# Performance work log

Hardware: AMD Instinct MI355X
Metric: run time of the kernel (lower is better)

Reference implementation:

```python
import jax, jax.numpy as jnp
import numpy as np

HS_LIST = [1024, 2048]   # hidden_size choices
IS_LIST = [2752, 5504]   # intermediate_size choices
A_BITS = [4, 8]
W_BITS = [4, 8]


def fake_quant(t, bits):
    # symmetric per-tensor fake quantization with straight-through estimator
    qmax = 2.0 ** (bits - 1) - 1.0
    s = jnp.maximum(jnp.max(jnp.abs(t)) / qmax, 1e-8)
    q = jnp.round(t / s) * s
    return t + jax.lax.stop_gradient(q - t)


def mixed_linear(inp, W, in_sizes, out_sizes, p_in, p_out, p_a, p_w):
    """Weight-entangled mixed-precision linear: weighted sum over the
    cartesian product of (in_size, out_size, a_bit, w_bit) choices.
    W has shape [max(out_sizes), max(in_sizes)]; sub-slices are shared."""
    out_max = max(out_sizes)
    acc = jnp.zeros(inp.shape[:-1] + (out_max,), inp.dtype)
    for i, cin in enumerate(in_sizes):
        x_sub = inp[..., :cin]
        for k, ab in enumerate(A_BITS):
            xq = fake_quant(x_sub, ab)
            for j, cout in enumerate(out_sizes):
                w_sub = W[:cout, :cin]
                for l, wb in enumerate(W_BITS):
                    wq = fake_quant(w_sub, wb)
                    y = jnp.einsum('bsh,oh->bso', xq, wq)
                    y = jnp.pad(y, ((0, 0), (0, 0), (0, out_max - cout)))
                    acc = acc + (p_in[i] * p_out[j] * p_a[k] * p_w[l]) * y
    return acc


def setup_inputs() -> dict:
    key = jax.random.key(0)
    ks = jax.random.split(key, 8)
    HS, IS = max(HS_LIST), max(IS_LIST)
    return {
        'x': jax.random.normal(ks[0], (1, 1024, HS), jnp.float32),
        'p_hidden': jax.random.normal(ks[1], (2,), jnp.float32),
        'p_inter': jax.random.normal(ks[2], (2,), jnp.float32),
        'p_abit': jax.random.normal(ks[3], (2,), jnp.float32),
        'p_wbit': jax.random.normal(ks[4], (2,), jnp.float32),
        'W_gate': jax.random.normal(ks[5], (IS, HS), jnp.float32) * 0.02,
        'W_up': jax.random.normal(ks[6], (IS, HS), jnp.float32) * 0.02,
        'W_down': jax.random.normal(ks[7], (HS, IS), jnp.float32) * 0.02,
    }


def reference(x, p_hidden, p_inter, p_abit, p_wbit, W_gate, W_up, W_down):
    # mixop softmaxes the architecture parameters into mixture probabilities
    wh = jax.nn.softmax(p_hidden)
    wi = jax.nn.softmax(p_inter)
    wa = jax.nn.softmax(p_abit)
    ww = jax.nn.softmax(p_wbit)
    x_up = mixed_linear(x, W_up, HS_LIST, IS_LIST, wh, wi, wa, ww)
    x_gate = jax.nn.silu(mixed_linear(x, W_gate, HS_LIST, IS_LIST, wh, wi, wa, ww))
    h = x_gate * x_up
    # down_proj (reverse=True): input dims are intermediate, output dims hidden;
    # op list is built over (intermediate, hidden) choices, weighted in the same
    # arch-param order (hidden probs pair with the first/intermediate choice axis).
    out = mixed_linear(h, W_down, IS_LIST, HS_LIST, wh, wi, wa, ww)
    return out
```

## Files before the change

kernel.cpp:

```cpp
#include <hip/hip_runtime.h>

typedef __attribute__((ext_vector_type(8))) short short8;
typedef __attribute__((ext_vector_type(4))) float f32x4;
typedef unsigned short u16;
typedef unsigned int u32;
typedef unsigned long long u64;

#define P_WH 0
#define P_WI 2
#define P_WA 4
#define P_WW 6
#define SL_AX 8
#define SL_WUP 12
#define SL_WGATE 16
#define SL_WDOWN 20
#define SL_AH 24
#define P_SX 28
#define P_SWUP 32
#define P_SWGATE 40
#define P_SWDOWN 48
#define P_SH 56

__device__ __forceinline__ u16 f2bf(float f) {
  u32 u = __float_as_uint(f);
  u = (u + 0x7FFFu + ((u >> 16) & 1u)) >> 16;
  return (u16)u;
}
__device__ __forceinline__ float bf2f(u16 h) { return __uint_as_float(((u32)h) << 16); }
__device__ __forceinline__ float fquant(float v, float s) { return rintf(v / s) * s; }

typedef const __attribute__((address_space(1))) u32 gl_u32;
typedef __attribute__((address_space(3))) u32 lds_u32;
__device__ __forceinline__ void gload_lds16(const void* g, void* l) {
  __builtin_amdgcn_global_load_lds((gl_u32*)g, (lds_u32*)l, 16, 0, 0);
}

#define WAITVM8()  asm volatile("s_waitcnt vmcnt(8)" ::: "memory")
#define WAITVM2()  asm volatile("s_waitcnt vmcnt(2)" ::: "memory")
#define WAITVM0()  asm volatile("s_waitcnt vmcnt(0)" ::: "memory")
#define BARRIER()  asm volatile("s_barrier" ::: "memory")

__global__ void k_init(const float* ph, const float* pi, const float* pa,
                       const float* pw, float* P) {
  if (threadIdx.x == 0) {
    u32* U = (u32*)P;
    for (int i = SL_AX; i < SL_AH + 2; ++i) U[i] = 0u;
    const float* src[4] = {ph, pi, pa, pw};
    #pragma unroll
    for (int t = 0; t < 4; ++t) {
      float a = src[t][0], b = src[t][1];
      float mx = fmaxf(a, b);
      float ea = expf(a - mx), eb = expf(b - mx);
      float s = ea + eb;
      P[t * 2 + 0] = ea / s;
      P[t * 2 + 1] = eb / s;
    }
  }
}

template <bool POW2>
__device__ __forceinline__ void amax_proc(float4 d, int v, u32 magic, int C,
                                          int r0, int c0,
                                          float& m0, float& m1, float& m2, float& m3) {
  int lin = v << 2;
  int o, c;
  if (POW2) { o = lin >> 11; c = lin & 2047; }
  else {
    o = (int)(((u64)(u32)lin * magic) >> 40);
    c = lin - o * C;
  }
  float mm = fmaxf(fmaxf(fabsf(d.x), fabsf(d.y)), fmaxf(fabsf(d.z), fabsf(d.w)));
  bool rlo = o < r0, clo = c < c0;
  m0 = fmaxf(m0, (rlo && clo) ? mm : 0.f);
  m1 = fmaxf(m1, (rlo && !clo) ? mm : 0.f);
  m2 = fmaxf(m2, (!rlo && clo) ? mm : 0.f);
  m3 = fmaxf(m3, (!rlo && !clo) ? mm : 0.f);
}

template <bool POW2>
__device__ __forceinline__ void absmax_dev(const float4* __restrict__ A4,
                                           int nvec, u32 magic, int C, int r0, int c0,
                                           int slotbase, float* P, int bid, int nb) {
  float m0 = 0.f, m1 = 0.f, m2 = 0.f, m3 = 0.f;
  const int tid = threadIdx.x;
  const int step = nb * 256;
  int v = bid * 256 + tid;
  for (; v + 3 * step < nvec; v += 4 * step) {
    float4 d0 = A4[v];
    float4 d1 = A4[v + step];
    float4 d2 = A4[v + 2 * step];
    float4 d3 = A4[v + 3 * step];
    amax_proc<POW2>(d0, v,            magic, C, r0, c0, m0, m1, m2, m3);
    amax_proc<POW2>(d1, v + step,     magic, C, r0, c0, m0, m1, m2, m3);
    amax_proc<POW2>(d2, v + 2 * step, magic, C, r0, c0, m0, m1, m2, m3);
    amax_proc<POW2>(d3, v + 3 * step, magic, C, r0, c0, m0, m1, m2, m3);
  }
  for (; v < nvec; v += step) {
    float4 d0 = A4[v];
    amax_proc<POW2>(d0, v, magic, C, r0, c0, m0, m1, m2, m3);
  }
  #pragma unroll
  for (int off = 32; off > 0; off >>= 1) {
    m0 = fmaxf(m0, __shfl_xor(m0, off));
    m1 = fmaxf(m1, __shfl_xor(m1, off));
    m2 = fmaxf(m2, __shfl_xor(m2, off));
    m3 = fmaxf(m3, __shfl_xor(m3, off));
  }
  __shared__ float red[16];
  const int wave = tid >> 6;
  if ((tid & 63) == 0) {
    red[wave * 4 + 0] = m0;
    red[wave * 4 + 1] = m1;
    red[wave * 4 + 2] = m2;
    red[wave * 4 + 3] = m3;
  }
  __syncthreads();
  if (tid < 4) {
    float mm = fmaxf(fmaxf(red[tid], red[4 + tid]), fmaxf(red[8 + tid], red[12 + tid]));
    if (mm > 0.f) atomicMax((u32*)P + slotbase + tid, __float_as_uint(mm));
  }
}

__global__ __launch_bounds__(256) void k_absmax4(const float* x, const float* Wu,
                                                 const float* Wg, const float* Wd,
                                                 u32 magic5504, float* P) {
  int b = blockIdx.x;
  if (b < 256)        absmax_dev<true >((const float4*)x,  (1024 * 2048) >> 2, 0, 2048, 1024, 1024, SL_AX,    P, b,        256);
  else if (b < 768)   absmax_dev<true >((const float4*)Wu, (5504 * 2048) >> 2, 0, 2048, 2752, 1024, SL_WUP,   P, b - 256,  512);
  else if (b < 1280)  absmax_dev<true >((const float4*)Wg, (5504 * 2048) >> 2, 0, 2048, 2752, 1024, SL_WGATE, P, b - 768,  512);
  else                absmax_dev<false>((const float4*)Wd, (2048 * 5504) >> 2, magic5504, 5504, 1024, 2752, SL_WDOWN, P, b - 1280, 512);
}

__global__ void k_params1(float* P) {
  if (threadIdx.x != 0 || blockIdx.x != 0) return;
  u32* U = (u32*)P;
  float x00 = __uint_as_float(U[SL_AX + 0]);
  float x01 = __uint_as_float(U[SL_AX + 1]);
  float ax0 = x00;
  float ax1 = fmaxf(x00, x01);
  P[P_SX + 0] = fmaxf(ax0 / 7.f, 1e-8f);
  P[P_SX + 1] = fmaxf(ax0 / 127.f, 1e-8f);
  P[P_SX + 2] = fmaxf(ax1 / 7.f, 1e-8f);
  P[P_SX + 3] = fmaxf(ax1 / 127.f, 1e-8f);
  const int sl[3] = {SL_WUP, SL_WGATE, SL_WDOWN};
  const int sb[3] = {P_SWUP, P_SWGATE, P_SWDOWN};
  #pragma unroll
  for (int t = 0; t < 3; ++t) {
    float q00 = __uint_as_float(U[sl[t] + 0]);
    float q01 = __uint_as_float(U[sl[t] + 1]);
    float q10 = __uint_as_float(U[sl[t] + 2]);
    float q11 = __uint_as_float(U[sl[t] + 3]);
    float a0 = q00;
    float a1 = fmaxf(q00, q10);
    float a2 = fmaxf(q00, q01);
    float a3 = fmaxf(fmaxf(q00, q01), fmaxf(q10, q11));
    float aa[4] = {a0, a1, a2, a3};
    #pragma unroll
    for (int ij = 0; ij < 4; ++ij) {
      P[sb[t] + ij * 2 + 0] = fmaxf(aa[ij] / 7.f, 1e-8f);
      P[sb[t] + ij * 2 + 1] = fmaxf(aa[ij] / 127.f, 1e-8f);
    }
  }
}

__global__ void k_params2(float* P) {
  if (threadIdx.x != 0 || blockIdx.x != 0) return;
  u32* U = (u32*)P;
  float a0 = __uint_as_float(U[SL_AH]);
  float a1 = fmaxf(a0, __uint_as_float(U[SL_AH + 1]));
  P[P_SH + 0] = fmaxf(a0 / 7.f, 1e-8f);
  P[P_SH + 1] = fmaxf(a0 / 127.f, 1e-8f);
  P[P_SH + 2] = fmaxf(a1 / 7.f, 1e-8f);
  P[P_SH + 3] = fmaxf(a1 / 127.f, 1e-8f);
}

__device__ __forceinline__ void build_x_one(
    const float* __restrict__ src, const float* __restrict__ P,
    u16* __restrict__ Xh, u16* __restrict__ Xl,
    int Csrc, int cin0, int K, int sbx, int gid, int kpr) {
  int row = gid / kpr;
  int kc_out = (gid - row * kpr) << 3;
  int kc_log = kc_out ^ (((row >> 1) & 3) << 3);
  int i = (kc_log >= cin0) ? 1 : 0;
  int c = kc_log - i * cin0;
  float pin = P[P_WH + i];
  float wa0 = P[P_WA], wa1 = P[P_WA + 1];
  float s4 = P[sbx + i * 2], s8 = P[sbx + i * 2 + 1];
  const float* sp = src + (size_t)row * Csrc + c;
  float v[8];
  *(float4*)&v[0] = *(const float4*)sp;
  *(float4*)&v[4] = *(const float4*)(sp + 4);
  short8 hv, lv;
  #pragma unroll
  for (int e = 0; e < 8; ++e) {
    float val = pin * (wa0 * fquant(v[e], s4) + wa1 * fquant(v[e], s8));
    u16 h = f2bf(val);
    hv[e] = (short)h;
    lv[e] = (short)f2bf(val - bf2f(h));
  }
  size_t off = (size_t)row * K + kc_out;
  *(short8*)(Xh + off) = hv;
  *(short8*)(Xl + off) = lv;
}

__device__ __forceinline__ void build_w_one(
    const float* __restrict__ W, const float* __restrict__ P,
    u16* __restrict__ Wh, u16* __restrict__ Wl,
    int Csrc, int cin0, int K, int sbw, int cout0, int rowoff,
    int gid, int kpr) {
  int row = gid / kpr;
  int kc_out = (gid - row * kpr) << 3;
  int kc_log = kc_out ^ (((row >> 1) & 3) << 3);
  int i = (kc_log >= cin0) ? 1 : 0;
  int c = kc_log - i * cin0;
  float wi0 = P[P_WI], wi1 = P[P_WI + 1];
  float ww0 = P[P_WW], ww1 = P[P_WW + 1];
  float s00 = P[sbw + i * 4 + 0];
  float s01 = P[sbw + i * 4 + 1];
  float s10 = P[sbw + i * 4 + 2];
  float s11 = P[sbw + i * 4 + 3];
  float keep0 = (row < cout0) ? wi0 : 0.f;
  const float* sp = W + (size_t)row * Csrc + c;
  float v[8];
  *(float4*)&v[0] = *(const float4*)sp;
  *(float4*)&v[4] = *(const float4*)(sp + 4);
  short8 hv, lv;
  #pragma unroll
  for (int e = 0; e < 8; ++e) {
    float w = v[e];
    float t0 = ww0 * fquant(w, s00) + ww1 * fquant(w, s01);
    float t1 = ww0 * fquant(w, s10) + ww1 * fquant(w, s11);
    float val = keep0 * t0 + wi1 * t1;
    u16 h = f2bf(val);
    hv[e] = (short)h;
    lv[e] = (short)f2bf(val - bf2f(h));
  }
  size_t off = (size_t)(row + rowoff) * K + kc_out;
  *(short8*)(Wh + off) = hv;
  *(short8*)(Wl + off) = lv;
}

__global__ __launch_bounds__(256) void k_build_x(
    const float* __restrict__ src, const float* __restrict__ P,
    u16* __restrict__ Xh, u16* __restrict__ Xl,
    int rows, int Csrc, int cin0, int K, int sbx) {
  int kpr = K >> 3;
  int nch = rows * kpr;
  int gid = blockIdx.x * blockDim.x + threadIdx.x;
  if (gid >= nch) return;
  build_x_one(src, P, Xh, Xl, Csrc, cin0, K, sbx, gid, kpr);
}

__global__ __launch_bounds__(256) void k_build_w(
    const float* __restrict__ W, const float* __restrict__ P,
    u16* __restrict__ Wh, u16* __restrict__ Wl,
    int R, int Csrc, int cin0, int K, int sbw, int cout0) {
  int kpr = K >> 3;
  int nch = R * kpr;
  int gid = blockIdx.x * blockDim.x + threadIdx.x;
  if (gid >= nch) return;
  build_w_one(W, P, Wh, Wl, Csrc, cin0, K, sbw, cout0, 0, gid, kpr);
}

__global__ __launch_bounds__(256) void k_build1(
    const float* __restrict__ x, const float* __restrict__ Wu,
    const float* __restrict__ Wg, const float* __restrict__ P,
    u16* __restrict__ X1h, u16* __restrict__ X1l,
    u16* __restrict__ Wh, u16* __restrict__ Wl) {
  int bid = blockIdx.x;
  if (bid < 1536) {
    int gid = bid * 256 + threadIdx.x;
    build_x_one(x, P, X1h, X1l, 2048, 1024, 3072, P_SX, gid, 384);
  } else {
    int gid = (bid - 1536) * 256 + threadIdx.x;
    const int nch = 5504 * 384;
    if (gid < nch)
      build_w_one(Wu, P, Wh, Wl, 2048, 1024, 3072, P_SWUP,   2752, 0,    gid,       384);
    else
      build_w_one(Wg, P, Wh, Wl, 2048, 1024, 3072, P_SWGATE, 2752, 5504, gid - nch, 384);
  }
}

__global__ __launch_bounds__(256) void k_build2(
    const float* __restrict__ H, const float* __restrict__ Wd,
    const float* __restrict__ P,
    u16* __restrict__ X2h, u16* __restrict__ X2l,
    u16* __restrict__ Wdh, u16* __restrict__ Wdl) {
  int bid = blockIdx.x;
  if (bid < 4128) {
    int gid = bid * 256 + threadIdx.x;
    build_x_one(H, P, X2h, X2l, 5504, 2752, 8256, P_SH, gid, 1032);
  } else {
    int gid = (bid - 4128) * 256 + threadIdx.x;
    build_w_one(Wd, P, Wdh, Wdl, 5504, 2752, 8256, P_SWDOWN, 1024, 0, gid, 1032);
  }
}

__global__ __launch_bounds__(256) void k_h(const float* __restrict__ U_,
                                           const float* __restrict__ G_,
                                           float* __restrict__ H_, float* P) {
  int nvec = (1024 * 5504) >> 2;
  int gstride = gridDim.x * blockDim.x;
  float m0 = 0.f, m1 = 0.f;
  for (int v = blockIdx.x * blockDim.x + threadIdx.x; v < nvec; v += gstride) {
    float4 u = ((const float4*)U_)[v];
    float4 g = ((const float4*)G_)[v];
    float4 h;
    h.x = u.x * (g.x / (1.f + expf(-g.x)));
    h.y = u.y * (g.y / (1.f + expf(-g.y)));
    h.z = u.z * (g.z / (1.f + expf(-g.z)));
    h.w = u.w * (g.w / (1.f + expf(-g.w)));
    ((float4*)H_)[v] = h;
    int c = (v << 2) % 5504;
    float mm = fmaxf(fmaxf(fabsf(h.x), fabsf(h.y)), fmaxf(fabsf(h.z), fabsf(h.w)));
    if (c < 2752) m0 = fmaxf(m0, mm); else m1 = fmaxf(m1, mm);
  }
  #pragma unroll
  for (int off = 32; off > 0; off >>= 1) {
    m0 = fmaxf(m0, __shfl_xor(m0, off));
    m1 = fmaxf(m1, __shfl_xor(m1, off));
  }
  if ((threadIdx.x & 63) == 0) {
    u32* slots = (u32*)P;
    if (m0 > 0.f) atomicMax(slots + SL_AH, __float_as_uint(m0));
    if (m1 > 0.f) atomicMax(slots + SL_AH + 1, __float_as_uint(m1));
  }
}

template <int MF, int NF>
__global__ __launch_bounds__(256) void k_gemm(
    const u16* __restrict__ Ah, const u16* __restrict__ Al,
    const u16* __restrict__ Bh, const u16* __restrict__ Bl,
    float* __restrict__ C0, float* __restrict__ C1, int nsplit, int ldc,
    int M, int N, int K) {
  constexpr int BM = MF * 32;
  constexpr int BN = NF * 32;
  constexpr int HALF = (2 * BM + 2 * BN) * 32;
  constexpr int nsegA = BM / 16;
  constexpr int nsegB = BN / 16;
  constexpr int NSEG = 2 * nsegA + 2 * nsegB;
  constexpr int NJ = NSEG / 4;
  static_assert(NJ == 8, "vmcnt immediates assume 8 loads per stage");
  __shared__ __align__(16) u16 S[2 * HALF];

  const int tid = threadIdx.x;
  const int wave = tid >> 6;
  const int lane = tid & 63;

  const int gx = gridDim.x;
  const int nwg = gx * gridDim.y;
  const int orig = blockIdx.y * gx + blockIdx.x;
  const int q = nwg >> 3, r = nwg & 7;
  const int xcd = orig & 7, linb = orig >> 3;
  const int swz = (xcd < r ? xcd * (q + 1) : r * (q + 1) + (xcd - r) * q) + linb;
  const int m0 = (swz % gx) * BM;
  const int n0 = (swz / gx) * BN;

  const int St = K >> 5;
  const int Z = gridDim.z;
  const int zb = St / Z, zr = St - zb * Z;
  const int z = blockIdx.z;
  const int nst = zb + ((z < zr) ? 1 : 0);
  const int k0 = (z * zb + ((z < zr) ? z : zr)) << 5;

  const int wr = wave >> 1, wc = wave & 1;
  const int lrow = lane >> 2;
  const int lcol = (lane & 3) << 3;
  const int fr = lane & 15;
  const int fq4 = (lane >> 4) << 2;
  const int kofs = (lane >> 4) << 3;

  f32x4 acc[MF][NF];
  #pragma unroll
  for (int m = 0; m < MF; ++m)
    #pragma unroll
    for (int n = 0; n < NF; ++n) acc[m][n] = (f32x4){0.f, 0.f, 0.f, 0.f};

  const u16* srcp[NJ];
  int loff[NJ];
  #pragma unroll
  for (int j = 0; j < NJ; ++j) {
    int g = j * 4 + wave;
    const u16* gb; int abase, trow, segi;
    if (g < nsegA)               { gb = Ah; abase = 0;                  trow = m0; segi = g; }
    else if (g < 2 * nsegA)      { gb = Al; abase = BM * 32;            trow = m0; segi = g - nsegA; }
    else if (g < 2 * nsegA + nsegB) { gb = Bh; abase = 2 * BM * 32;     trow = n0; segi = g - 2 * nsegA; }
    else                         { gb = Bl; abase = 2 * BM * 32 + BN * 32; trow = n0; segi = g - 2 * nsegA - nsegB; }
    srcp[j] = gb + (size_t)(trow + segi * 16 + lrow) * K + (k0 + lcol);
    loff[j] = abase + segi * 512;
  }

  int aoh[MF], aol[MF], boh[NF], bol[NF];
  #pragma unroll
  for (int m = 0; m < MF; ++m) {
    int rr = wr * (MF * 16) + m * 16 + fr;
    int idx = rr * 32 + (kofs ^ (((rr >> 1) & 3) << 3));
    aoh[m] = idx;
    aol[m] = BM * 32 + idx;
  }
  #pragma unroll
  for (int n = 0; n < NF; ++n) {
    int rr = wc * (NF * 16) + n * 16 + fr;
    int idx = rr * 32 + (kofs ^ (((rr >> 1) & 3) << 3));
    boh[n] = 2 * BM * 32 + idx;
    bol[n] = 2 * BM * 32 + BN * 32 + idx;
  }

  #define STAGE(bufo)                                           \
    { _Pragma("unroll")                                         \
      for (int j = 0; j < NJ; ++j) {                            \
        gload_lds16(srcp[j], S + (bufo) + loff[j]);             \
        srcp[j] += 32;                                          \
      } }

  #define COMPUTE(bufo)                                                         \
    { short8 afh[MF], afl[MF], bfh[NF], bfl[NF];                                \
      _Pragma("unroll")                                                         \
      for (int m = 0; m < MF; ++m) {                                            \
        afh[m] = *(const short8*)(S + (bufo) + aoh[m]);                         \
        afl[m] = *(const short8*)(S + (bufo) + aol[m]);                         \
      }                                                                         \
      _Pragma("unroll")                                                         \
      for (int n = 0; n < NF; ++n) {                                            \
        bfh[n] = *(const short8*)(S + (bufo) + boh[n]);                         \
        bfl[n] = *(const short8*)(S + (bufo) + bol[n]);                         \
      }                                                                         \
      _Pragma("unroll")                                                         \
      for (int m = 0; m < MF; ++m)                                              \
        _Pragma("unroll")                                                       \
        for (int n = 0; n < NF; ++n) {                                          \
          acc[m][n] = __builtin_amdgcn_mfma_f32_16x16x32_bf16(afh[m], bfh[n], acc[m][n], 0, 0, 0); \
          acc[m][n] = __builtin_amdgcn_mfma_f32_16x16x32_bf16(afh[m], bfl[n], acc[m][n], 0, 0, 0); \
          acc[m][n] = __builtin_amdgcn_mfma_f32_16x16x32_bf16(afl[m], bfh[n], acc[m][n], 0, 0, 0); \
        } }

  int curo = 0;
  STAGE(curo);
  for (int t = 0; t + 1 < nst; ++t) {
    STAGE(curo ^ HALF);
    WAITVM8();
    BARRIER();
    COMPUTE(curo);
    BARRIER();
    curo ^= HALF;
  }
  WAITVM0();
  BARRIER();
  COMPUTE(curo);

  #undef STAGE
  #undef COMPUTE

  float* base = (n0 < nsplit) ? C0 : C1;
  const int ncol0 = (n0 < nsplit) ? 0 : nsplit;
  float* Cz = base + (size_t)z * M * ldc;
  #pragma unroll
  for (int m = 0; m < MF; ++m) {
    #pragma unroll
    for (int n = 0; n < NF; ++n) {
      int row = m0 + wr * (MF * 16) + m * 16 + fq4;
      int col = n0 + wc * (NF * 16) + n * 16 + fr - ncol0;
      float* cp = Cz + (size_t)row * ldc + col;
      f32x4 a = acc[m][n];
      cp[0] = a[0];
      cp[(size_t)ldc] = a[1];
      cp[(size_t)2 * ldc] = a[2];
      cp[(size_t)3 * ldc] = a[3];
    }
  }
}

template <int CMODE>
__global__ __launch_bounds__(512) void k_gemm8w(
    const u16* __restrict__ Ah, const u16* __restrict__ Al,
    const u16* __restrict__ Bh, const u16* __restrict__ Bl,
    float* __restrict__ C0, float* __restrict__ C1, int nsplit, int ldc,
    int M, int N, int K) {
  constexpr int BM = 256, BN = 256;
  constexpr int HALF = (2 * BM + 2 * BN) * 32;
  constexpr int NJ = 8;
  __shared__ __align__(16) u16 S[2 * HALF];

  const int tid = threadIdx.x;
  const int wave = tid >> 6;
  const int lane = tid & 63;

  const int gx = gridDim.x;
  const int nwg = gx * gridDim.y;
  const int orig = blockIdx.y * gx + blockIdx.x;
  const int q = nwg >> 3, r = nwg & 7;
  const int xcd = orig & 7, linb = orig >> 3;
  const int swz = (xcd < r ? xcd * (q + 1) : r * (q + 1) + (xcd - r) * q) + linb;
  const int m0 = (swz % gx) * BM;
  const int n0 = (swz / gx) * BN;

  const int St = K >> 5;
  const int Z = gridDim.z;
  const int zb = St / Z, zr = St - zb * Z;
  const int z = blockIdx.z;
  const int nst = zb + ((z < zr) ? 1 : 0);
  const int k0 = (z * zb + ((z < zr) ? z : zr)) << 5;

  const int wr = wave >> 2;
  const int wc = wave & 3;
  const int lrow = lane >> 2;
  const int lcol = (lane & 3) << 3;
  const int fr = lane & 15;
  const int fq4 = (lane >> 4) << 2;
  const int kofs = (lane >> 4) << 3;
  const int kx = kofs ^ (((fr >> 1) & 3) << 3);

  f32x4 acc[8][4];
  #pragma unroll
  for (int m = 0; m < 8; ++m)
    #pragma unroll
    for (int n = 0; n < 4; ++n) acc[m][n] = (f32x4){0.f, 0.f, 0.f, 0.f};

  const u16* srcp[NJ];
  int loff[NJ];
  #pragma unroll
  for (int j = 0; j < NJ; ++j) {
    int g = j * 8 + wave;
    const u16* gb; int abase, trow, segi;
    if (g < 16)      { gb = Ah; abase = 0;         trow = m0; segi = g; }
    else if (g < 32) { gb = Al; abase = 8192;      trow = m0; segi = g - 16; }
    else if (g < 48) { gb = Bh; abase = 16384;     trow = n0; segi = g - 32; }
    else             { gb = Bl; abase = 24576;     trow = n0; segi = g - 48; }
    srcp[j] = gb + (size_t)(trow + segi * 16 + lrow) * K + (k0 + lcol);
    loff[j] = abase + segi * 512;
  }

  const int aoh0 = (wr * 128 + fr) * 32 + kx;
  const int aol0 = 8192 + aoh0;
  const int boh0 = 16384 + (wc * 64 + fr) * 32 + kx;
  const int bol0 = boh0 + 8192;

  #define ISSUE2(bufo, j0)                                             \
    { gload_lds16(srcp[j0], S + (bufo) + loff[j0]);  srcp[j0] += 32;   \
      gload_lds16(srcp[j0+1], S + (bufo) + loff[j0+1]); srcp[j0+1] += 32; }

  int curo = 0;
  ISSUE2(curo, 0); ISSUE2(curo, 2); ISSUE2(curo, 4); ISSUE2(curo, 6);

  for (int t = 0; t < nst; ++t) {
    const int nxt = curo ^ HALF;
    const bool more = (t + 1 < nst);
    if (more) { ISSUE2(nxt, 0); WAITVM2(); } else { WAITVM0(); }
    BARRIER();

    short8 bh_[4], bl_[4];
    #pragma unroll
    for (int p = 0; p < 4; ++p) {
      const int m2 = 2 * p;
      short8 a0h = *(const short8*)(S + curo + aoh0 + m2 * 512);
      short8 a0l = *(const short8*)(S + curo + aol0 + m2 * 512);
      short8 a1h = *(const short8*)(S + curo + aoh0 + (m2 + 1) * 512);
      short8 a1l = *(const short8*)(S + curo + aol0 + (m2 + 1) * 512);
      if (p == 0) {
        #pragma unroll
        for (int n = 0; n < 4; ++n) {
          bh_[n] = *(const short8*)(S + curo + boh0 + n * 512);
          bl_[n] = *(const short8*)(S + curo + bol0 + n * 512);
        }
      }
      if (more) {
        if (p == 0) { ISSUE2(nxt, 2); }
        else if (p == 1) { ISSUE2(nxt, 4); }
        else if (p == 2) { ISSUE2(nxt, 6); }
      }
      BARRIER();
      __builtin_amdgcn_s_setprio(1);
      #pragma unroll
      for (int n = 0; n < 4; ++n) {
        acc[m2][n] = __builtin_amdgcn_mfma_f32_16x16x32_bf16(a0h, bh_[n], acc[m2][n], 0, 0, 0);
        acc[m2][n] = __builtin_amdgcn_mfma_f32_16x16x32_bf16(a0h, bl_[n], acc[m2][n], 0, 0, 0);
        acc[m2][n] = __builtin_amdgcn_mfma_f32_16x16x32_bf16(a0l, bh_[n], acc[m2][n], 0, 0, 0);
        acc[m2+1][n] = __builtin_amdgcn_mfma_f32_16x16x32_bf16(a1h, bh_[n], acc[m2+1][n], 0, 0, 0);
        acc[m2+1][n] = __builtin_amdgcn_mfma_f32_16x16x32_bf16(a1h, bl_[n], acc[m2+1][n], 0, 0, 0);
        acc[m2+1][n] = __builtin_amdgcn_mfma_f32_16x16x32_bf16(a1l, bh_[n], acc[m2+1][n], 0, 0, 0);
      }
      __builtin_amdgcn_s_setprio(0);
      BARRIER();
    }
    curo ^= HALF;
  }
  #undef ISSUE2

  if (CMODE == 0) {
    #pragma unroll
    for (int m = 0; m < 8; ++m) {
      #pragma unroll
      for (int n = 0; n < 4; ++n) {
        int row = m0 + wr * 128 + m * 16 + fq4;
        int col = n0 + wc * 64 + n * 16 + fr;
        float* base = (col < nsplit) ? C0 : C1;
        int cw = (col < nsplit) ? col : col - nsplit;
        float* cp = base + (size_t)row * ldc + cw;
        f32x4 a = acc[m][n];
        cp[0] = a[0];
        cp[(size_t)ldc] = a[1];
        cp[(size_t)2 * ldc] = a[2];
        cp[(size_t)3 * ldc] = a[3];
      }
    }
  } else {
    float* Cz = (z < 4) ? (C0 + (size_t)z * M * ldc) : (C1 + (size_t)(z - 4) * M * ldc);
    #pragma unroll
    for (int m = 0; m < 8; ++m) {
      #pragma unroll
      for (int n = 0; n < 4; ++n) {
        int row = m0 + wr * 128 + m * 16 + fq4;
        int col = n0 + wc * 64 + n * 16 + fr;
        float* cp = Cz + (size_t)row * ldc + col;
        f32x4 a = acc[m][n];
        cp[0] = a[0];
        cp[(size_t)ldc] = a[1];
        cp[(size_t)2 * ldc] = a[2];
        cp[(size_t)3 * ldc] = a[3];
      }
    }
  }
}

__global__ __launch_bounds__(256) void k_reduce8(const float4* __restrict__ p0,
                                                 const float4* __restrict__ p1,
                                                 float4* __restrict__ out, int nvec) {
  int stride = gridDim.x * blockDim.x;
  for (int i = blockIdx.x * blockDim.x + threadIdx.x; i < nvec; i += stride) {
    float4 s = p0[i];
    #pragma unroll
    for (int zz = 1; zz < 4; ++zz) {
      float4 b = p0[(size_t)zz * nvec + i];
      s.x += b.x; s.y += b.y; s.z += b.z; s.w += b.w;
    }
    #pragma unroll
    for (int zz = 0; zz < 4; ++zz) {
      float4 b = p1[(size_t)zz * nvec + i];
      s.x += b.x; s.y += b.y; s.z += b.z; s.w += b.w;
    }
    out[i] = s;
  }
}

__global__ __launch_bounds__(256) void k_reduce4(const float4* __restrict__ p,
                                                 float4* __restrict__ out, int nvec) {
  int stride = gridDim.x * blockDim.x;
  for (int i = blockIdx.x * blockDim.x + threadIdx.x; i < nvec; i += stride) {
    float4 a = p[i], b = p[nvec + i], c = p[2 * nvec + i], d = p[3 * nvec + i];
    float4 o;
    o.x = ((a.x + b.x) + c.x) + d.x;
    o.y = ((a.y + b.y) + c.y) + d.y;
    o.z = ((a.z + b.z) + c.z) + d.z;
    o.w = ((a.w + b.w) + c.w) + d.w;
    out[i] = o;
  }
}

extern "C" void kernel_launch(void* const* d_in, const int* in_sizes, int n_in,
                              void* d_out, int out_size, void* d_ws, size_t ws_size,
                              hipStream_t stream) {
  const float* x  = (const float*)d_in[0];
  const float* ph = (const float*)d_in[1];
  const float* pi = (const float*)d_in[2];
  const float* pa = (const float*)d_in[3];
  const float* pw = (const float*)d_in[4];
  const float* Wg = (const float*)d_in[5];
  const float* Wu = (const float*)d_in[6];
  const float* Wd = (const float*)d_in[7];
  float* out = (float*)d_out;

  const u32 magic5504 = (u32)(((1ULL << 40) + 5503ULL) / 5504ULL);
  char* ws = (char*)d_ws;

  const size_t szX1 = (size_t)1024 * 3072 * 2;
  const size_t szWug = (size_t)11008 * 3072 * 2;
  const size_t szUP = (size_t)1024 * 5504 * 4;
  const size_t fused_need = 1024 + 2 * szX1 + 2 * szWug + 2 * szUP;

  if (ws_size >= fused_need) {
    size_t off = 0;
    float* P = (float*)(ws + off); off += 1024;
    u16* X1h = (u16*)(ws + off); off += szX1;
    u16* X1l = (u16*)(ws + off); off += szX1;
    u16* Wh  = (u16*)(ws + off); off += szWug;
    u16* Wl  = (u16*)(ws + off); off += szWug;
    float* UP   = (float*)(ws + off); off += szUP;
    float* GATE = (float*)(ws + off); off += szUP;
    float* H = UP;
    u16* X2h = Wh;
    u16* X2l = Wh + (size_t)1024 * 8256;
    float* DPz1 = (float*)(Wh + (size_t)2 * 1024 * 8256);
    float* DPz0 = UP;
    u16* Wdh = Wl;
    u16* Wdl = Wl + (size_t)2048 * 8256;

    k_init<<<1, 64, 0, stream>>>(ph, pi, pa, pw, P);
    k_absmax4<<<1792, 256, 0, stream>>>(x, Wu, Wg, Wd, magic5504, P);
    k_params1<<<1, 64, 0, stream>>>(P);

    k_build1<<<1536 + 16512, 256, 0, stream>>>(x, Wu, Wg, P, X1h, X1l, Wh, Wl);

    dim3 g1(1024 / 256, 11008 / 256, 1);
    k_gemm8w<0><<<g1, 512, 0, stream>>>(X1h, X1l, Wh, Wl, UP, GATE, 5504, 5504,
                                        1024, 11008, 3072);

    k_h<<<2048, 256, 0, stream>>>(UP, GATE, H, P);
    k_params2<<<1, 64, 0, stream>>>(P);

    k_build2<<<4128 + 8256, 256, 0, stream>>>(H, Wd, P, X2h, X2l, Wdh, Wdl);

    dim3 g2(1024 / 256, 2048 / 256, 8);
    k_gemm8w<1><<<g2, 512, 0, stream>>>(X2h, X2l, Wdh, Wdl, DPz0, DPz1, 2048, 2048,
                                        1024, 2048, 8256);
    k_reduce8<<<2048, 256, 0, stream>>>((const float4*)DPz0, (const float4*)DPz1,
                                        (float4*)out, (1024 * 2048) / 4);
    return;
  }

  size_t off = 0;
  float* P = (float*)(ws + off); off += 1024;
  u16* X1h = (u16*)(ws + off); off += szX1;
  u16* X1l = (u16*)(ws + off); off += szX1;
  u16* Wh  = (u16*)(ws + off); off += (size_t)5504 * 3072 * 2;
  u16* Wl  = (u16*)(ws + off); off += (size_t)5504 * 3072 * 2;
  float* UP   = (float*)(ws + off); off += (size_t)1024 * 5504 * 4;
  float* GATE = (float*)(ws + off); off += (size_t)1024 * 5504 * 4;
  u16* X2h = (u16*)(ws + off); off += (size_t)1024 * 8256 * 2;
  u16* X2l = (u16*)(ws + off); off += (size_t)1024 * 8256 * 2;
  float* H = UP;
  float* DPART = UP;
  if (ws_size < off) return;

  k_init<<<1, 64, 0, stream>>>(ph, pi, pa, pw, P);
  k_absmax4<<<1792, 256, 0, stream>>>(x, Wu, Wg, Wd, magic5504, P);
  k_params1<<<1, 64, 0, stream>>>(P);

  {
    int nch = 1024 * (3072 / 8);
    k_build_x<<<(nch + 255) / 256, 256, 0, stream>>>(x, P, X1h, X1l, 1024, 2048, 1024, 3072, P_SX);
  }
  {
    int nch = 5504 * (3072 / 8);
    k_build_w<<<(nch + 255) / 256, 256, 0, stream>>>(Wu, P, Wh, Wl, 5504, 2048, 1024, 3072, P_SWUP, 2752);
  }
  dim3 g1(1024 / 128, 5504 / 128, 1);
  k_gemm<4, 4><<<g1, 256, 0, stream>>>(X1h, X1l, Wh, Wl, UP, UP, 5504, 5504, 1024, 5504, 3072);
  {
    int nch = 5504 * (3072 / 8);
    k_build_w<<<(nch + 255) / 256, 256, 0, stream>>>(Wg, P, Wh, Wl, 5504, 2048, 1024, 3072, P_SWGATE, 2752);
  }
  k_gemm<4, 4><<<g1, 256, 0, stream>>>(X1h, X1l, Wh, Wl, GATE, GATE, 5504, 5504, 1024, 5504, 3072);

  k_h<<<2048, 256, 0, stream>>>(UP, GATE, H, P);
  k_params2<<<1, 64, 0, stream>>>(P);

  {
    int nch = 1024 * (8256 / 8);
    k_build_x<<<(nch + 255) / 256, 256, 0, stream>>>(H, P, X2h, X2l, 1024, 5504, 2752, 8256, P_SH);
  }
  {
    int nch = 2048 * (8256 / 8);
    k_build_w<<<(nch + 255) / 256, 256, 0, stream>>>(Wd, P, Wh, Wl, 2048, 5504, 2752, 8256, P_SWDOWN, 1024);
  }
  dim3 g2(1024 / 128, 2048 / 128, 4);
  k_gemm<4, 4><<<g2, 256, 0, stream>>>(X2h, X2l, Wh, Wl, DPART, DPART, 2048, 2048, 1024, 2048, 8256);
  k_reduce4<<<2048, 256, 0, stream>>>((const float4*)DPART, (float4*)out, (1024 * 2048) / 4);
}
```

Before: 576.1 us.

## Fuse SiLU-gating and abs-max into up/gate GEMM epilogue via interleaved weight rows

Interleaves the up and gate weight rows in 16-row groups when building the packed weight matrix, so each GEMM wave holds matching up and gate accumulator tiles side by side. A new epilogue mode computes h = up * silu(gate) directly from the accumulators, writes H, and reduces the per-half abs-max with wave shuffles and atomicMax. This drops the separate k_h pass and the full fp32 round trip of UP and GATE through global memory. The cost is expf work and atomics in the GEMM epilogue, and the workspace layout is reshuffled, with a dedicated buffer for the down-projection partials.

```diff
diff --git a/kernel.cpp b/kernel.cpp
--- a/kernel.cpp
+++ b/kernel.cpp
@@ -206,11 +206,9 @@
 __device__ __forceinline__ void build_w_one(
     const float* __restrict__ W, const float* __restrict__ P,
     u16* __restrict__ Wh, u16* __restrict__ Wl,
-    int Csrc, int cin0, int K, int sbw, int cout0, int rowoff,
-    int gid, int kpr) {
-  int row = gid / kpr;
-  int kc_out = (gid - row * kpr) << 3;
-  int kc_log = kc_out ^ (((row >> 1) & 3) << 3);
+    int Csrc, int cin0, int K, int sbw, int cout0,
+    int row_src, int row_store, int kc_out) {
+  int kc_log = kc_out ^ (((row_store >> 1) & 3) << 3);
   int i = (kc_log >= cin0) ? 1 : 0;
   int c = kc_log - i * cin0;
   float wi0 = P[P_WI], wi1 = P[P_WI + 1];
@@ -219,8 +217,8 @@
   float s01 = P[sbw + i * 4 + 1];
   float s10 = P[sbw + i * 4 + 2];
   float s11 = P[sbw + i * 4 + 3];
-  float keep0 = (row < cout0) ? wi0 : 0.f;
-  const float* sp = W + (size_t)row * Csrc + c;
+  float keep0 = (row_src < cout0) ? wi0 : 0.f;
+  const float* sp = W + (size_t)row_src * Csrc + c;
   float v[8];
   *(float4*)&v[0] = *(const float4*)sp;
   *(float4*)&v[4] = *(const float4*)(sp + 4);
@@ -235,7 +233,7 @@
     hv[e] = (short)h;
     lv[e] = (short)f2bf(val - bf2f(h));
   }
-  size_t off = (size_t)(row + rowoff) * K + kc_out;
+  size_t off = (size_t)row_store * K + kc_out;
   *(short8*)(Wh + off) = hv;
   *(short8*)(Wl + off) = lv;
 }
@@ -259,7 +257,9 @@
   int nch = R * kpr;
   int gid = blockIdx.x * blockDim.x + threadIdx.x;
   if (gid >= nch) return;
-  build_w_one(W, P, Wh, Wl, Csrc, cin0, K, sbw, cout0, 0, gid, kpr);
+  int row = gid / kpr;
+  int kc_out = (gid - row * kpr) << 3;
+  build_w_one(W, P, Wh, Wl, Csrc, cin0, K, sbw, cout0, row, row, kc_out);
 }
 
 __global__ __launch_bounds__(256) void k_build1(
@@ -274,10 +274,15 @@
   } else {
     int gid = (bid - 1536) * 256 + threadIdx.x;
     const int nch = 5504 * 384;
-    if (gid < nch)
-      build_w_one(Wu, P, Wh, Wl, 2048, 1024, 3072, P_SWUP,   2752, 0,    gid,       384);
+    bool isg = gid >= nch;
+    int g2 = isg ? gid - nch : gid;
+    int row = g2 / 384;
+    int kc_out = (g2 - row * 384) << 3;
+    int row_store = (((row >> 4) << 5) + (row & 15)) + (isg ? 16 : 0);
+    if (!isg)
+      build_w_one(Wu, P, Wh, Wl, 2048, 1024, 3072, P_SWUP,   2752, row, row_store, kc_out);
     else
-      build_w_one(Wg, P, Wh, Wl, 2048, 1024, 3072, P_SWGATE, 2752, 5504, gid - nch, 384);
+      build_w_one(Wg, P, Wh, Wl, 2048, 1024, 3072, P_SWGATE, 2752, row, row_store, kc_out);
   }
 }
 
@@ -292,7 +297,9 @@
     build_x_one(H, P, X2h, X2l, 5504, 2752, 8256, P_SH, gid, 1032);
   } else {
     int gid = (bid - 4128) * 256 + threadIdx.x;
-    build_w_one(Wd, P, Wdh, Wdl, 5504, 2752, 8256, P_SWDOWN, 1024, 0, gid, 1032);
+    int row = gid / 1032;
+    int kc_out = (gid - row * 1032) << 3;
+    build_w_one(Wd, P, Wdh, Wdl, 5504, 2752, 8256, P_SWDOWN, 1024, row, row, kc_out);
   }
 }
 
@@ -586,22 +593,37 @@
   }
   #undef ISSUE2
 
-  if (CMODE == 0) {
-    #pragma unroll
-    for (int m = 0; m < 8; ++m) {
+  if (CMODE == 2) {
+    float hm0 = 0.f, hm1 = 0.f;
+    #pragma unroll
+    for (int nn = 0; nn < 2; ++nn) {
+      const int n = nn * 2;
+      int lcol2 = (((n0 + wc * 64 + n * 16) >> 5) << 4) + fr;
+      bool lo = lcol2 < 2752;
       #pragma unroll
-      for (int n = 0; n < 4; ++n) {
+      for (int m = 0; m < 8; ++m) {
         int row = m0 + wr * 128 + m * 16 + fq4;
-        int col = n0 + wc * 64 + n * 16 + fr;
-        float* base = (col < nsplit) ? C0 : C1;
-        int cw = (col < nsplit) ? col : col - nsplit;
-        float* cp = base + (size_t)row * ldc + cw;
-        f32x4 a = acc[m][n];
-        cp[0] = a[0];
-        cp[(size_t)ldc] = a[1];
-        cp[(size_t)2 * ldc] = a[2];
-        cp[(size_t)3 * ldc] = a[3];
+        float* hp = C0 + (size_t)row * ldc + lcol2;
+        f32x4 au = acc[m][n], ag = acc[m][n + 1];
+        #pragma unroll
+        for (int j = 0; j < 4; ++j) {
+          float g = ag[j];
+          float h = au[j] * (g / (1.f + expf(-g)));
+          hp[(size_t)j * ldc] = h;
+          float a = fabsf(h);
+          if (lo) hm0 = fmaxf(hm0, a); else hm1 = fmaxf(hm1, a);
+        }
       }
+    }
+    #pragma unroll
+    for (int off = 32; off > 0; off >>= 1) {
+      hm0 = fmaxf(hm0, __shfl_xor(hm0, off));
+      hm1 = fmaxf(hm1, __shfl_xor(hm1, off));
+    }
+    if (lane == 0) {
+      u32* slots = (u32*)C1;
+      if (hm0 > 0.f) atomicMax(slots + SL_AH, __float_as_uint(hm0));
+      if (hm1 > 0.f) atomicMax(slots + SL_AH + 1, __float_as_uint(hm1));
     }
   } else {
     float* Cz = (z < 4) ? (C0 + (size_t)z * M * ldc) : (C1 + (size_t)(z - 4) * M * ldc);
@@ -674,8 +696,9 @@
 
   const size_t szX1 = (size_t)1024 * 3072 * 2;
   const size_t szWug = (size_t)11008 * 3072 * 2;
-  const size_t szUP = (size_t)1024 * 5504 * 4;
-  const size_t fused_need = 1024 + 2 * szX1 + 2 * szWug + 2 * szUP;
+  const size_t szH = (size_t)1024 * 5504 * 4;
+  const size_t szDP = (size_t)4 * 1024 * 2048 * 4;
+  const size_t fused_need = 1024 + 2 * szX1 + 2 * szWug + szH + szDP;
 
   if (ws_size >= fused_need) {
     size_t off = 0;
@@ -684,13 +707,11 @@
     u16* X1l = (u16*)(ws + off); off += szX1;
     u16* Wh  = (u16*)(ws + off); off += szWug;
     u16* Wl  = (u16*)(ws + off); off += szWug;
-    float* UP   = (float*)(ws + off); off += szUP;
-    float* GATE = (float*)(ws + off); off += szUP;
-    float* H = UP;
+    float* H = (float*)(ws + off); off += szH;
+    float* DPz0 = (float*)(ws + off); off += szDP;
     u16* X2h = Wh;
     u16* X2l = Wh + (size_t)1024 * 8256;
     float* DPz1 = (float*)(Wh + (size_t)2 * 1024 * 8256);
-    float* DPz0 = UP;
     u16* Wdh = Wl;
     u16* Wdl = Wl + (size_t)2048 * 8256;
 
@@ -701,10 +722,9 @@
     k_build1<<<1536 + 16512, 256, 0, stream>>>(x, Wu, Wg, P, X1h, X1l, Wh, Wl);
 
     dim3 g1(1024 / 256, 11008 / 256, 1);
-    k_gemm8w<0><<<g1, 512, 0, stream>>>(X1h, X1l, Wh, Wl, UP, GATE, 5504, 5504,
+    k_gemm8w<2><<<g1, 512, 0, stream>>>(X1h, X1l, Wh, Wl, H, P, 5504, 5504,
                                         1024, 11008, 3072);
 
-    k_h<<<2048, 256, 0, stream>>>(UP, GATE, H, P);
     k_params2<<<1, 64, 0, stream>>>(P);
 
     k_build2<<<4128 + 8256, 256, 0, stream>>>(H, Wd, P, X2h, X2l, Wdh, Wdl);
```

Result: faster. 473.7 us, median of 2 (-17.8%).
